# Kernel optimization log

Hardware: AMD Instinct MI355X
Metric: run time of the kernel (lower is better)

## Reference

```python
import jax, jax.numpy as jnp
import numpy as np

N = 20000
E = 640000
IN_DIM = 128
HID = 128
OUT = 64


def setup_inputs() -> dict:
    key = jax.random.key(0)
    ks = jax.random.split(key, 16)
    s = 0.05
    inp = {
        'feat': jax.random.normal(ks[0], (N, IN_DIM), jnp.float32),
        'edge_index': jax.random.randint(ks[1], (2, E), 0, N, jnp.int64),
        # GCNConv params
        'W_gcn': jax.random.normal(ks[2], (IN_DIM, HID), jnp.float32) * s,
        'b_gcn': jnp.zeros((HID,), jnp.float32),
        # SAGEConv params (lin_l: aggregated neighbors w/ bias; lin_r: root, no bias)
        'W_sage_l': jax.random.normal(ks[3], (HID, HID), jnp.float32) * s,
        'b_sage_l': jnp.zeros((HID,), jnp.float32),
        'W_sage_r': jax.random.normal(ks[4], (HID, HID), jnp.float32) * s,
        # policy MLP
        'W1': jax.random.normal(ks[5], (HID, HID), jnp.float32) * s,
        'b1': jnp.zeros((HID,), jnp.float32),
        'W2': jax.random.normal(ks[6], (HID, HID), jnp.float32) * s,
        'b2': jnp.zeros((HID,), jnp.float32),
        'W3': jax.random.normal(ks[7], (HID, OUT), jnp.float32) * s,
        'b3': jnp.zeros((OUT,), jnp.float32),
        # value head
        'Wv': jax.random.normal(ks[8], (HID, 1), jnp.float32) * s,
        'bv': jnp.zeros((1,), jnp.float32),
    }
    return inp


def _gcn(feat, src, dst, W, b):
    # PyG GCNConv: add self loops, sym-normalize by deg^-1/2 on both ends
    loop = jnp.arange(N, dtype=src.dtype)
    s = jnp.concatenate([src, loop])
    d = jnp.concatenate([dst, loop])
    deg = jax.ops.segment_sum(jnp.ones_like(d, jnp.float32), d, num_segments=N)
    dinv = jnp.where(deg > 0, jax.lax.rsqrt(deg), 0.0)
    x = feat @ W  # [N, HID]
    msg = x[s] * (dinv[s] * dinv[d])[:, None]  # [E+N, HID]
    return jax.ops.segment_sum(msg, d, num_segments=N) + b


def _sage_mean(h, src, dst, Wl, bl, Wr):
    # PyG SAGEConv(aggr='mean'): lin_l(mean_neigh) + lin_r(root)
    neigh_sum = jax.ops.segment_sum(h[src], dst, num_segments=N)
    cnt = jax.ops.segment_sum(jnp.ones_like(dst, jnp.float32), dst, num_segments=N)
    mean = neigh_sum / jnp.maximum(cnt, 1.0)[:, None]
    return mean @ Wl + bl + h @ Wr


def reference(feat, edge_index, W_gcn, b_gcn, W_sage_l, b_sage_l, W_sage_r,
              W1, b1, W2, b2, W3, b3, Wv, bv):
    src, dst = edge_index[0], edge_index[1]
    h = jax.nn.relu(_gcn(feat, src, dst, W_gcn, b_gcn))
    h = jax.nn.relu(_sage_mean(h, src, dst, W_sage_l, b_sage_l, W_sage_r))
    # policy MLP (GELU exact, matching torch nn.GELU default)
    z = jax.nn.gelu(h @ W1 + b1, approximate=False)
    z = jax.nn.gelu(z @ W2 + b2, approximate=False)
    means = z @ W3 + b3  # [N, OUT]
    values = (h @ Wv + bv)[:, 0]  # [N]
    return (means, values)
```

## Files before the change

kernel.cpp:

```cpp
#include <hip/hip_runtime.h>
#include <math.h>


typedef __attribute__((ext_vector_type(8))) short short8;
typedef __attribute__((ext_vector_type(4))) float floatx4;

__device__ __forceinline__ unsigned short f2b(float f) {
    unsigned u = __float_as_uint(f);
    unsigned r = (u + 0x7fffu + ((u >> 16) & 1u)) >> 16;
    return (unsigned short)r;
}
__device__ __forceinline__ float b2f(unsigned short h) {
    return __uint_as_float(((unsigned)h) << 16);
}
__device__ __forceinline__ float b2f_lo(unsigned v) {
    return __uint_as_float(v << 16);
}
__device__ __forceinline__ float b2f_hi(unsigned v) {
    return __uint_as_float(v & 0xffff0000u);
}
__device__ __forceinline__ floatx4 MFMA(short8 a, short8 b, floatx4 c) {
    return __builtin_amdgcn_mfma_f32_16x16x32_bf16(a, b, c, 0, 0, 0);
}
__device__ __forceinline__ float gelu_exact(float x) {
    return 0.5f * x * (1.0f + erff(x * 0.70710678118654752440f));
}

#define FRAG(P, ct, ks, lane) (*(const short8*)((P) + (((((ct)*4 + (ks))*64) + (lane)) << 3)))


__global__ __launch_bounds__(256) void count_pack_kernel(
    const int* __restrict__ eidx, int E,
    int* __restrict__ cnt, int* __restrict__ rank,
    const float* Wg, const float* Wsl, const float* Wsr,
    const float* W1, const float* W2, const float* W3,
    unsigned short* Pg, unsigned short* Psl, unsigned short* Psr,
    unsigned short* P1, unsigned short* P2, unsigned short* P3,
    int countBlocks)
{
    if ((int)blockIdx.x < countBlocks) {
        int e = blockIdx.x * 256 + threadIdx.x;
        if (e < E) {
            int d = eidx[E + e];
            rank[e] = atomicAdd(&cnt[d], 1);
        }
        return;
    }
    int t = (blockIdx.x - countBlocks) * 256 + threadIdx.x;
    const float* W; unsigned short* P; int NC = 128; int base;
    if (t < 2048)       { W = Wg;  P = Pg;  base = t; }
    else if (t < 4096)  { W = Wsl; P = Psl; base = t - 2048; }
    else if (t < 6144)  { W = Wsr; P = Psr; base = t - 4096; }
    else if (t < 8192)  { W = W1;  P = P1;  base = t - 6144; }
    else if (t < 10240) { W = W2;  P = P2;  base = t - 8192; }
    else if (t < 11264) { W = W3;  P = P3;  base = t - 10240; NC = 64; }
    else return;
    int l  = base & 63;
    int ks = (base >> 6) & 3;
    int ct = base >> 8;
    int n  = ct * 16 + (l & 15);
    int k0 = ks * 32 + ((l >> 4) << 3);
    short8 v;
    #pragma unroll
    for (int j = 0; j < 8; j++) v[j] = (short)f2b(W[(size_t)(k0 + j) * NC + n]);
    *(short8*)(P + ((size_t)base << 3)) = v;
}


__global__ __launch_bounds__(256) void scan_kernel(
    const int* __restrict__ cnt, int N,
    int* __restrict__ row_ptr, int* __restrict__ bsums,
    float* __restrict__ dinv)
{
    __shared__ int sh[256];
    int b = blockIdx.x, tid = threadIdx.x;
    int i0 = b * 1024 + tid * 4;
    int v0 = (i0 + 0 < N) ? cnt[i0 + 0] : 0;
    int v1 = (i0 + 1 < N) ? cnt[i0 + 1] : 0;
    int v2 = (i0 + 2 < N) ? cnt[i0 + 2] : 0;
    int v3 = (i0 + 3 < N) ? cnt[i0 + 3] : 0;
    int tot = v0 + v1 + v2 + v3;
    sh[tid] = tot;
    __syncthreads();
    for (int off = 1; off < 256; off <<= 1) {
        int t = (tid >= off) ? sh[tid - off] : 0;
        __syncthreads();
        sh[tid] += t;
        __syncthreads();
    }
    int excl = sh[tid] - tot;
    if (i0 + 0 < N) { row_ptr[i0 + 0] = excl;                dinv[i0 + 0] = rsqrtf((float)(v0 + 1)); }
    if (i0 + 1 < N) { row_ptr[i0 + 1] = excl + v0;           dinv[i0 + 1] = rsqrtf((float)(v1 + 1)); }
    if (i0 + 2 < N) { row_ptr[i0 + 2] = excl + v0 + v1;      dinv[i0 + 2] = rsqrtf((float)(v2 + 1)); }
    if (i0 + 3 < N) { row_ptr[i0 + 3] = excl + v0 + v1 + v2; dinv[i0 + 3] = rsqrtf((float)(v3 + 1)); }
    if (tid == 255) bsums[b] = sh[255];
}


__global__ __launch_bounds__(256) void fill_gemm_kernel(
    const int* __restrict__ eidx, const int* __restrict__ rank,
    const int* __restrict__ row_ptr, const int* __restrict__ bsums,
    int E, int* __restrict__ col,
    const float* __restrict__ feat, const unsigned short* __restrict__ Pg,
    unsigned short* __restrict__ xs, int M, int fillBlocks)
{
    if ((int)blockIdx.x < fillBlocks) {
        int e = blockIdx.x * 256 + threadIdx.x;
        if (e < E) {
            int d = eidx[E + e];
            int b = d >> 10;
            int off = 0;
            for (int j = 0; j < b; j++) off += bsums[j];
            col[off + row_ptr[d] + rank[e]] = eidx[e];
        }
        return;
    }
    int bid = blockIdx.x - fillBlocks;
    int w = bid * 4 + (threadIdx.x >> 6);
    if (w >= (M / 16) * 2) return;
    int lane = threadIdx.x & 63;
    int m = lane & 15, quad = lane >> 4;
    int rt = w >> 1, ch = w & 1;
    const float* arow = feat + (size_t)(rt * 16 + m) * 128;
    short8 a[4];
    #pragma unroll
    for (int ks = 0; ks < 4; ks++) {
        float4 f0 = *(const float4*)(arow + ks * 32 + quad * 8);
        float4 f1 = *(const float4*)(arow + ks * 32 + quad * 8 + 4);
        short8 s;
        s[0] = (short)f2b(f0.x); s[1] = (short)f2b(f0.y);
        s[2] = (short)f2b(f0.z); s[3] = (short)f2b(f0.w);
        s[4] = (short)f2b(f1.x); s[5] = (short)f2b(f1.y);
        s[6] = (short)f2b(f1.z); s[7] = (short)f2b(f1.w);
        a[ks] = s;
    }
    #pragma unroll
    for (int ct = 0; ct < 4; ct++) {
        floatx4 acc = {0.f, 0.f, 0.f, 0.f};
        #pragma unroll
        for (int ks = 0; ks < 4; ks++)
            acc = MFMA(a[ks], FRAG(Pg, ch * 4 + ct, ks, lane), acc);
        #pragma unroll
        for (int reg = 0; reg < 4; reg++)
            xs[(size_t)(rt * 16 + quad * 4 + reg) * 128 + (ch * 4 + ct) * 16 + m] =
                f2b(acc[reg]);
    }
}


template<bool GCN>
__global__ __launch_bounds__(256) void agg_kernel(
    const unsigned short* __restrict__ X, const int* __restrict__ row_ptr,
    const int* __restrict__ bsums, const int* __restrict__ col,
    const float* __restrict__ dinv, const float* __restrict__ bias,
    unsigned short* __restrict__ Y, int N, int E)
{
    int w = (int)((blockIdx.x * 256 + threadIdx.x) >> 6);
    if (w >= N) return;
    int lane = threadIdx.x & 63;
    int g = lane >> 4, t = lane & 15;
    const uint4* Xq = (const uint4*)X;

    int b = w >> 10;
    int off = 0;
    for (int j = 0; j < b; j++) off += bsums[j];
    int beg = off + row_ptr[w];
    int end;
    if (w + 1 < N) {
        int off2 = (((w + 1) >> 10) != b) ? off + bsums[b] : off;
        end = off2 + row_ptr[w + 1];
    } else end = E;
    int deg = end - beg;

    float acc[8] = {0.f, 0.f, 0.f, 0.f, 0.f, 0.f, 0.f, 0.f};

    for (int base = beg; base < end; base += 64) {
        int rem = end - base;
        int n = rem < 64 ? rem : 64;
        int idx = (lane < n) ? col[base + lane] : 0;
        for (int j0 = 0; j0 < n; j0 += 16) {
            #pragma unroll
            for (int u = 0; u < 4; u++) {
                int j = j0 + u * 4 + g;
                int s = __shfl(idx, j & 63);
                if (j < n) {
                    uint4 q = Xq[(size_t)s * 16 + t];
                    float sc = GCN ? dinv[s] : 1.0f;
                    acc[0] = fmaf(b2f_lo(q.x), sc, acc[0]);
                    acc[1] = fmaf(b2f_hi(q.x), sc, acc[1]);
                    acc[2] = fmaf(b2f_lo(q.y), sc, acc[2]);
                    acc[3] = fmaf(b2f_hi(q.y), sc, acc[3]);
                    acc[4] = fmaf(b2f_lo(q.z), sc, acc[4]);
                    acc[5] = fmaf(b2f_hi(q.z), sc, acc[5]);
                    acc[6] = fmaf(b2f_lo(q.w), sc, acc[6]);
                    acc[7] = fmaf(b2f_hi(q.w), sc, acc[7]);
                }
            }
        }
    }
    #pragma unroll
    for (int i = 0; i < 8; i++) {
        acc[i] += __shfl_xor(acc[i], 16);
        acc[i] += __shfl_xor(acc[i], 32);
    }
    if (g == 0) {
        float out[8];
        if (GCN) {
            float dw = dinv[w];
            uint4 q = Xq[(size_t)w * 16 + t];
            acc[0] = fmaf(b2f_lo(q.x), dw, acc[0]);
            acc[1] = fmaf(b2f_hi(q.x), dw, acc[1]);
            acc[2] = fmaf(b2f_lo(q.y), dw, acc[2]);
            acc[3] = fmaf(b2f_hi(q.y), dw, acc[3]);
            acc[4] = fmaf(b2f_lo(q.z), dw, acc[4]);
            acc[5] = fmaf(b2f_hi(q.z), dw, acc[5]);
            acc[6] = fmaf(b2f_lo(q.w), dw, acc[6]);
            acc[7] = fmaf(b2f_hi(q.w), dw, acc[7]);
            float4 b0 = *(const float4*)(bias + t * 8);
            float4 b1 = *(const float4*)(bias + t * 8 + 4);
            out[0] = fmaxf(fmaf(acc[0], dw, b0.x), 0.f);
            out[1] = fmaxf(fmaf(acc[1], dw, b0.y), 0.f);
            out[2] = fmaxf(fmaf(acc[2], dw, b0.z), 0.f);
            out[3] = fmaxf(fmaf(acc[3], dw, b0.w), 0.f);
            out[4] = fmaxf(fmaf(acc[4], dw, b1.x), 0.f);
            out[5] = fmaxf(fmaf(acc[5], dw, b1.y), 0.f);
            out[6] = fmaxf(fmaf(acc[6], dw, b1.z), 0.f);
            out[7] = fmaxf(fmaf(acc[7], dw, b1.w), 0.f);
        } else {
            float rc = 1.0f / (float)(deg > 0 ? deg : 1);
            #pragma unroll
            for (int i = 0; i < 8; i++) out[i] = acc[i] * rc;
        }
        uint4 r;
        r.x = (unsigned)f2b(out[0]) | ((unsigned)f2b(out[1]) << 16);
        r.y = (unsigned)f2b(out[2]) | ((unsigned)f2b(out[3]) << 16);
        r.z = (unsigned)f2b(out[4]) | ((unsigned)f2b(out[5]) << 16);
        r.w = (unsigned)f2b(out[6]) | ((unsigned)f2b(out[7]) << 16);
        ((uint4*)Y)[(size_t)w * 16 + t] = r;
    }
}


__global__ __launch_bounds__(256) void sage_mlp_kernel(
    const unsigned short* __restrict__ mean, const unsigned short* __restrict__ h1,
    const unsigned short* __restrict__ Psl, const unsigned short* __restrict__ Psr,
    const float* __restrict__ bsl,
    const unsigned short* __restrict__ P1, const float* __restrict__ b1,
    const unsigned short* __restrict__ P2, const float* __restrict__ b2,
    const unsigned short* __restrict__ P3, const float* __restrict__ b3,
    const float* __restrict__ Wv, const float* __restrict__ bv,
    float* __restrict__ means, float* __restrict__ values, int M)
{
    __shared__ unsigned short z[4][16 * 136];
    int widx = threadIdx.x >> 6, lane = threadIdx.x & 63;
    int w = blockIdx.x * 4 + widx;
    if (w >= M / 16) return;
    int m = lane & 15, quad = lane >> 4;
    unsigned short* zt = &z[widx][0];
    int r0 = w * 16;

    short8 am[4], ar[4];
    #pragma unroll
    for (int ks = 0; ks < 4; ks++) {
        am[ks] = *(const short8*)(mean + (size_t)(r0 + m) * 128 + ks * 32 + quad * 8);
        ar[ks] = *(const short8*)(h1   + (size_t)(r0 + m) * 128 + ks * 32 + quad * 8);
    }

    float vpart[4] = {0.f, 0.f, 0.f, 0.f};
    #pragma unroll
    for (int ct = 0; ct < 8; ct++) {
        floatx4 acc = {0.f, 0.f, 0.f, 0.f};
        #pragma unroll
        for (int ks = 0; ks < 4; ks++) acc = MFMA(am[ks], FRAG(Psl, ct, ks, lane), acc);
        #pragma unroll
        for (int ks = 0; ks < 4; ks++) acc = MFMA(ar[ks], FRAG(Psr, ct, ks, lane), acc);
        float bb = bsl[ct * 16 + m];
        float wv = Wv[ct * 16 + m];
        #pragma unroll
        for (int reg = 0; reg < 4; reg++) {
            float o = fmaxf(acc[reg] + bb, 0.f);
            vpart[reg] = fmaf(o, wv, vpart[reg]);
            zt[(quad * 4 + reg) * 136 + ct * 16 + m] = f2b(o);
        }
    }
    #pragma unroll
    for (int off = 1; off <= 8; off <<= 1) {
        #pragma unroll
        for (int reg = 0; reg < 4; reg++)
            vpart[reg] += __shfl_xor(vpart[reg], off);
    }
    if (m == 0) {
        float bvv = bv[0];
        #pragma unroll
        for (int reg = 0; reg < 4; reg++)
            values[r0 + quad * 4 + reg] = vpart[reg] + bvv;
    }

    short8 a1[4];
    #pragma unroll
    for (int ks = 0; ks < 4; ks++)
        a1[ks] = *(const short8*)(zt + m * 136 + ks * 32 + quad * 8);

    #pragma unroll
    for (int ct = 0; ct < 8; ct++) {
        floatx4 acc = {0.f, 0.f, 0.f, 0.f};
        #pragma unroll
        for (int ks = 0; ks < 4; ks++) acc = MFMA(a1[ks], FRAG(P1, ct, ks, lane), acc);
        float bb = b1[ct * 16 + m];
        #pragma unroll
        for (int reg = 0; reg < 4; reg++)
            zt[(quad * 4 + reg) * 136 + ct * 16 + m] = f2b(gelu_exact(acc[reg] + bb));
    }
    short8 a2[4];
    #pragma unroll
    for (int ks = 0; ks < 4; ks++)
        a2[ks] = *(const short8*)(zt + m * 136 + ks * 32 + quad * 8);

    #pragma unroll
    for (int ct = 0; ct < 8; ct++) {
        floatx4 acc = {0.f, 0.f, 0.f, 0.f};
        #pragma unroll
        for (int ks = 0; ks < 4; ks++) acc = MFMA(a2[ks], FRAG(P2, ct, ks, lane), acc);
        float bb = b2[ct * 16 + m];
        #pragma unroll
        for (int reg = 0; reg < 4; reg++)
            zt[(quad * 4 + reg) * 136 + ct * 16 + m] = f2b(gelu_exact(acc[reg] + bb));
    }
    short8 a3[4];
    #pragma unroll
    for (int ks = 0; ks < 4; ks++)
        a3[ks] = *(const short8*)(zt + m * 136 + ks * 32 + quad * 8);

    #pragma unroll
    for (int ct = 0; ct < 4; ct++) {
        floatx4 acc = {0.f, 0.f, 0.f, 0.f};
        #pragma unroll
        for (int ks = 0; ks < 4; ks++) acc = MFMA(a3[ks], FRAG(P3, ct, ks, lane), acc);
        float bb = b3[ct * 16 + m];
        #pragma unroll
        for (int reg = 0; reg < 4; reg++)
            means[(size_t)(r0 + quad * 4 + reg) * 64 + ct * 16 + m] = acc[reg] + bb;
    }
}


extern "C" void kernel_launch(void* const* d_in, const int* in_sizes, int n_in,
                              void* d_out, int out_size, void* d_ws, size_t ws_size,
                              hipStream_t stream) {
    const float* feat  = (const float*)d_in[0];
    const int*   eidx  = (const int*)d_in[1];
    const float* W_gcn = (const float*)d_in[2];
    const float* b_gcn = (const float*)d_in[3];
    const float* W_sl  = (const float*)d_in[4];
    const float* b_sl  = (const float*)d_in[5];
    const float* W_sr  = (const float*)d_in[6];
    const float* W1    = (const float*)d_in[7];
    const float* b1    = (const float*)d_in[8];
    const float* W2    = (const float*)d_in[9];
    const float* b2    = (const float*)d_in[10];
    const float* W3    = (const float*)d_in[11];
    const float* b3    = (const float*)d_in[12];
    const float* Wv    = (const float*)d_in[13];
    const float* bv    = (const float*)d_in[14];

    const int N = in_sizes[0] / 128;
    const int E = in_sizes[1] / 2;

    char* ws = (char*)d_ws;
    size_t off = 0;
    auto alloc = [&](size_t bytes) -> void* {
        void* p = ws + off;
        off += (bytes + 255) & ~(size_t)255;
        return p;
    };
    int*   cnt     = (int*)alloc((size_t)N * 4);
    int*   rank    = (int*)alloc((size_t)E * 4);
    int*   row_ptr = (int*)alloc((size_t)N * 4);
    int*   bsums   = (int*)alloc(32 * 4);
    float* dinv    = (float*)alloc((size_t)N * 4);
    int*   col     = (int*)alloc((size_t)E * 4);
    unsigned short* xs   = (unsigned short*)alloc((size_t)N * 128 * 2);
    unsigned short* h1   = (unsigned short*)alloc((size_t)N * 128 * 2);
    unsigned short* mean = (unsigned short*)alloc((size_t)N * 128 * 2);
    unsigned short* Pg   = (unsigned short*)alloc(2048 * 8 * 2);
    unsigned short* Psl  = (unsigned short*)alloc(2048 * 8 * 2);
    unsigned short* Psr  = (unsigned short*)alloc(2048 * 8 * 2);
    unsigned short* P1   = (unsigned short*)alloc(2048 * 8 * 2);
    unsigned short* P2   = (unsigned short*)alloc(2048 * 8 * 2);
    unsigned short* P3   = (unsigned short*)alloc(1024 * 8 * 2);

    hipMemsetAsync(cnt, 0, (size_t)N * 4, stream);

    const int countBlocks = (E + 255) / 256;
    const int packBlocks  = (11264 + 255) / 256;
    count_pack_kernel<<<countBlocks + packBlocks, 256, 0, stream>>>(
        eidx, E, cnt, rank, W_gcn, W_sl, W_sr, W1, W2, W3,
        Pg, Psl, Psr, P1, P2, P3, countBlocks);

    const int NB = (N + 1023) / 1024;
    scan_kernel<<<NB, 256, 0, stream>>>(cnt, N, row_ptr, bsums, dinv);

    const int fillBlocks = (E + 255) / 256;
    const int gemmBlocks = ((N / 16) * 2 + 3) / 4;
    fill_gemm_kernel<<<fillBlocks + gemmBlocks, 256, 0, stream>>>(
        eidx, rank, row_ptr, bsums, E, col, feat, Pg, xs, N, fillBlocks);

    const int agrid = (N + 3) / 4;
    agg_kernel<true><<<agrid, 256, 0, stream>>>(xs, row_ptr, bsums, col, dinv, b_gcn, h1, N, E);
    agg_kernel<false><<<agrid, 256, 0, stream>>>(h1, row_ptr, bsums, col, dinv, nullptr, mean, N, E);

    sage_mlp_kernel<<<(N / 16 + 3) / 4, 256, 0, stream>>>(
        mean, h1, Psl, Psr, b_sl, P1, b1, P2, b2, P3, b3, Wv, bv,
        (float*)d_out, (float*)d_out + (size_t)N * 64, N);
}
```

Before: 200.5 us.

## Rework CSR build with decoupled scan, partitioned atomic fill, prescaled GCN features

The per-edge rank array is replaced by atomic write pointers during CSR fill. The fill is partitioned into 8 destination ranges so that each block's atomics hit a localized region. The scan now uses a decoupled lookback with global flags to produce absolute row_ptr, which removes the bsums prefix loops in fill and aggregation. GCN features are prescaled by dinv[src] in the GEMM, so aggregation does plain adds with four independent gathers per iteration. The costs are that the fill reads the edge list 8 times and the column order within each row becomes nondeterministic. The scan's spin-wait also relies on earlier blocks making forward progress.

```diff
diff --git a/kernel.cpp b/kernel.cpp
--- a/kernel.cpp
+++ b/kernel.cpp
@@ -10,9 +10,6 @@
     unsigned r = (u + 0x7fffu + ((u >> 16) & 1u)) >> 16;
     return (unsigned short)r;
 }
-__device__ __forceinline__ float b2f(unsigned short h) {
-    return __uint_as_float(((unsigned)h) << 16);
-}
 __device__ __forceinline__ float b2f_lo(unsigned v) {
     return __uint_as_float(v << 16);
 }
@@ -30,8 +27,7 @@
 
 
 __global__ __launch_bounds__(256) void count_pack_kernel(
-    const int* __restrict__ eidx, int E,
-    int* __restrict__ cnt, int* __restrict__ rank,
+    const int* __restrict__ eidx, int E, int* __restrict__ cnt,
     const float* Wg, const float* Wsl, const float* Wsr,
     const float* W1, const float* W2, const float* W3,
     unsigned short* Pg, unsigned short* Psl, unsigned short* Psr,
@@ -40,10 +36,7 @@
 {
     if ((int)blockIdx.x < countBlocks) {
         int e = blockIdx.x * 256 + threadIdx.x;
-        if (e < E) {
-            int d = eidx[E + e];
-            rank[e] = atomicAdd(&cnt[d], 1);
-        }
+        if (e < E) atomicAdd(&cnt[eidx[E + e]], 1);
         return;
     }
     int t = (blockIdx.x - countBlocks) * 256 + threadIdx.x;
@@ -69,10 +62,11 @@
 
 __global__ __launch_bounds__(256) void scan_kernel(
     const int* __restrict__ cnt, int N,
-    int* __restrict__ row_ptr, int* __restrict__ bsums,
-    float* __restrict__ dinv)
+    int* __restrict__ row_ptr, int* __restrict__ wptr, float* __restrict__ dinv,
+    int* __restrict__ gflags, int* __restrict__ gsums)
 {
     __shared__ int sh[256];
+    __shared__ int s_off;
     int b = blockIdx.x, tid = threadIdx.x;
     int i0 = b * 1024 + tid * 4;
     int v0 = (i0 + 0 < N) ? cnt[i0 + 0] : 0;
@@ -88,30 +82,51 @@
         sh[tid] += t;
         __syncthreads();
     }
-    int excl = sh[tid] - tot;
-    if (i0 + 0 < N) { row_ptr[i0 + 0] = excl;                dinv[i0 + 0] = rsqrtf((float)(v0 + 1)); }
-    if (i0 + 1 < N) { row_ptr[i0 + 1] = excl + v0;           dinv[i0 + 1] = rsqrtf((float)(v1 + 1)); }
-    if (i0 + 2 < N) { row_ptr[i0 + 2] = excl + v0 + v1;      dinv[i0 + 2] = rsqrtf((float)(v2 + 1)); }
-    if (i0 + 3 < N) { row_ptr[i0 + 3] = excl + v0 + v1 + v2; dinv[i0 + 3] = rsqrtf((float)(v3 + 1)); }
-    if (tid == 255) bsums[b] = sh[255];
+    if (tid == 255) {
+        gsums[b] = sh[255];
+        __hip_atomic_store(&gflags[b], 1, __ATOMIC_RELEASE, __HIP_MEMORY_SCOPE_AGENT);
+    }
+    if (tid == 0) {
+        int off = 0;
+        for (int j = 0; j < b; j++) {
+            while (__hip_atomic_load(&gflags[j], __ATOMIC_ACQUIRE,
+                                     __HIP_MEMORY_SCOPE_AGENT) == 0) {}
+            off += gsums[j];
+        }
+        s_off = off;
+    }
+    __syncthreads();
+    int excl = s_off + sh[tid] - tot;
+    if (i0 + 0 < N) { row_ptr[i0 + 0] = excl;                wptr[i0 + 0] = excl;                dinv[i0 + 0] = rsqrtf((float)(v0 + 1)); }
+    if (i0 + 1 < N) { row_ptr[i0 + 1] = excl + v0;           wptr[i0 + 1] = excl + v0;           dinv[i0 + 1] = rsqrtf((float)(v1 + 1)); }
+    if (i0 + 2 < N) { row_ptr[i0 + 2] = excl + v0 + v1;      wptr[i0 + 2] = excl + v0 + v1;      dinv[i0 + 2] = rsqrtf((float)(v2 + 1)); }
+    if (i0 + 3 < N) { row_ptr[i0 + 3] = excl + v0 + v1 + v2; wptr[i0 + 3] = excl + v0 + v1 + v2; dinv[i0 + 3] = rsqrtf((float)(v3 + 1)); }
+    if (b == (int)gridDim.x - 1 && tid == 255) row_ptr[N] = s_off + sh[255];
 }
 
 
 __global__ __launch_bounds__(256) void fill_gemm_kernel(
-    const int* __restrict__ eidx, const int* __restrict__ rank,
-    const int* __restrict__ row_ptr, const int* __restrict__ bsums,
-    int E, int* __restrict__ col,
-    const float* __restrict__ feat, const unsigned short* __restrict__ Pg,
-    unsigned short* __restrict__ xs, int M, int fillBlocks)
+    const int* __restrict__ eidx, int E, int N,
+    int* __restrict__ wptr, int* __restrict__ col,
+    const float* __restrict__ feat, const float* __restrict__ dinv,
+    const unsigned short* __restrict__ Pg, unsigned short* __restrict__ xs,
+    int M, int fillBlocks, int PS)
 {
     if ((int)blockIdx.x < fillBlocks) {
-        int e = blockIdx.x * 256 + threadIdx.x;
-        if (e < E) {
-            int d = eidx[E + e];
-            int b = d >> 10;
-            int off = 0;
-            for (int j = 0; j < b; j++) off += bsums[j];
-            col[off + row_ptr[d] + rank[e]] = eidx[e];
+        int p = blockIdx.x & 7;
+        int chunk = blockIdx.x >> 3;
+        int dlo = p * PS;
+        int dhi = dlo + PS; if (dhi > N) dhi = N;
+        #pragma unroll
+        for (int it = 0; it < 8; it++) {
+            int e = (chunk * 8 + it) * 256 + threadIdx.x;
+            if (e < E) {
+                int d = eidx[E + e];
+                if (d >= dlo && d < dhi) {
+                    int pos = atomicAdd(&wptr[d], 1);
+                    col[pos] = eidx[e];
+                }
+            }
         }
         return;
     }
@@ -134,6 +149,9 @@
         s[6] = (short)f2b(f1.z); s[7] = (short)f2b(f1.w);
         a[ks] = s;
     }
+    float dvr[4];
+    #pragma unroll
+    for (int reg = 0; reg < 4; reg++) dvr[reg] = dinv[rt * 16 + quad * 4 + reg];
     #pragma unroll
     for (int ct = 0; ct < 4; ct++) {
         floatx4 acc = {0.f, 0.f, 0.f, 0.f};
@@ -143,59 +161,50 @@
         #pragma unroll
         for (int reg = 0; reg < 4; reg++)
             xs[(size_t)(rt * 16 + quad * 4 + reg) * 128 + (ch * 4 + ct) * 16 + m] =
-                f2b(acc[reg]);
-    }
-}
-
+                f2b(acc[reg] * dvr[reg]);
+    }
+}
+
+
+#define ACCUM(q)                                   \
+    acc[0] += b2f_lo((q).x); acc[1] += b2f_hi((q).x); \
+    acc[2] += b2f_lo((q).y); acc[3] += b2f_hi((q).y); \
+    acc[4] += b2f_lo((q).z); acc[5] += b2f_hi((q).z); \
+    acc[6] += b2f_lo((q).w); acc[7] += b2f_hi((q).w);
 
 template<bool GCN>
 __global__ __launch_bounds__(256) void agg_kernel(
     const unsigned short* __restrict__ X, const int* __restrict__ row_ptr,
-    const int* __restrict__ bsums, const int* __restrict__ col,
-    const float* __restrict__ dinv, const float* __restrict__ bias,
-    unsigned short* __restrict__ Y, int N, int E)
+    const int* __restrict__ col, const float* __restrict__ dinv,
+    const float* __restrict__ bias, unsigned short* __restrict__ Y, int N)
 {
     int w = (int)((blockIdx.x * 256 + threadIdx.x) >> 6);
     if (w >= N) return;
     int lane = threadIdx.x & 63;
     int g = lane >> 4, t = lane & 15;
     const uint4* Xq = (const uint4*)X;
-
-    int b = w >> 10;
-    int off = 0;
-    for (int j = 0; j < b; j++) off += bsums[j];
-    int beg = off + row_ptr[w];
-    int end;
-    if (w + 1 < N) {
-        int off2 = (((w + 1) >> 10) != b) ? off + bsums[b] : off;
-        end = off2 + row_ptr[w + 1];
-    } else end = E;
+    int beg = row_ptr[w], end = row_ptr[w + 1];
     int deg = end - beg;
 
     float acc[8] = {0.f, 0.f, 0.f, 0.f, 0.f, 0.f, 0.f, 0.f};
-
-    for (int base = beg; base < end; base += 64) {
-        int rem = end - base;
-        int n = rem < 64 ? rem : 64;
-        int idx = (lane < n) ? col[base + lane] : 0;
-        for (int j0 = 0; j0 < n; j0 += 16) {
-            #pragma unroll
-            for (int u = 0; u < 4; u++) {
-                int j = j0 + u * 4 + g;
-                int s = __shfl(idx, j & 63);
-                if (j < n) {
-                    uint4 q = Xq[(size_t)s * 16 + t];
-                    float sc = GCN ? dinv[s] : 1.0f;
-                    acc[0] = fmaf(b2f_lo(q.x), sc, acc[0]);
-                    acc[1] = fmaf(b2f_hi(q.x), sc, acc[1]);
-                    acc[2] = fmaf(b2f_lo(q.y), sc, acc[2]);
-                    acc[3] = fmaf(b2f_hi(q.y), sc, acc[3]);
-                    acc[4] = fmaf(b2f_lo(q.z), sc, acc[4]);
-                    acc[5] = fmaf(b2f_hi(q.z), sc, acc[5]);
-                    acc[6] = fmaf(b2f_lo(q.w), sc, acc[6]);
-                    acc[7] = fmaf(b2f_hi(q.w), sc, acc[7]);
-                }
-            }
+    int jb = beg;
+    for (; jb + 16 <= end; jb += 16) {
+        int s0 = col[jb + g];
+        int s1 = col[jb + g + 4];
+        int s2 = col[jb + g + 8];
+        int s3 = col[jb + g + 12];
+        uint4 q0 = Xq[(size_t)s0 * 16 + t];
+        uint4 q1 = Xq[(size_t)s1 * 16 + t];
+        uint4 q2 = Xq[(size_t)s2 * 16 + t];
+        uint4 q3 = Xq[(size_t)s3 * 16 + t];
+        ACCUM(q0) ACCUM(q1) ACCUM(q2) ACCUM(q3)
+    }
+    for (; jb < end; jb += 4) {
+        int j = jb + g;
+        if (j < end) {
+            int s = col[j];
+            uint4 q = Xq[(size_t)s * 16 + t];
+            ACCUM(q)
         }
     }
     #pragma unroll
@@ -206,16 +215,9 @@
     if (g == 0) {
         float out[8];
         if (GCN) {
+            uint4 q = Xq[(size_t)w * 16 + t];
+            ACCUM(q)
             float dw = dinv[w];
-            uint4 q = Xq[(size_t)w * 16 + t];
-            acc[0] = fmaf(b2f_lo(q.x), dw, acc[0]);
-            acc[1] = fmaf(b2f_hi(q.x), dw, acc[1]);
-            acc[2] = fmaf(b2f_lo(q.y), dw, acc[2]);
-            acc[3] = fmaf(b2f_hi(q.y), dw, acc[3]);
-            acc[4] = fmaf(b2f_lo(q.z), dw, acc[4]);
-            acc[5] = fmaf(b2f_hi(q.z), dw, acc[5]);
-            acc[6] = fmaf(b2f_lo(q.w), dw, acc[6]);
-            acc[7] = fmaf(b2f_hi(q.w), dw, acc[7]);
             float4 b0 = *(const float4*)(bias + t * 8);
             float4 b1 = *(const float4*)(bias + t * 8 + 4);
             out[0] = fmaxf(fmaf(acc[0], dw, b0.x), 0.f);
@@ -373,10 +375,12 @@
         off += (bytes + 255) & ~(size_t)255;
         return p;
     };
-    int*   cnt     = (int*)alloc((size_t)N * 4);
-    int*   rank    = (int*)alloc((size_t)E * 4);
-    int*   row_ptr = (int*)alloc((size_t)N * 4);
-    int*   bsums   = (int*)alloc(32 * 4);
+    int*   gflags  = (int*)alloc((size_t)(64 + N) * 4);
+    int*   cnt     = gflags + 64;
+    size_t zbytes  = (size_t)(64 + N) * 4;
+    int*   gsums   = (int*)alloc(64 * 4);
+    int*   row_ptr = (int*)alloc((size_t)(N + 1) * 4);
+    int*   wptr    = (int*)alloc((size_t)N * 4);
     float* dinv    = (float*)alloc((size_t)N * 4);
     int*   col     = (int*)alloc((size_t)E * 4);
     unsigned short* xs   = (unsigned short*)alloc((size_t)N * 128 * 2);
@@ -389,25 +393,27 @@
     unsigned short* P2   = (unsigned short*)alloc(2048 * 8 * 2);
     unsigned short* P3   = (unsigned short*)alloc(1024 * 8 * 2);
 
-    hipMemsetAsync(cnt, 0, (size_t)N * 4, stream);
+    hipMemsetAsync(gflags, 0, zbytes, stream);
 
     const int countBlocks = (E + 255) / 256;
     const int packBlocks  = (11264 + 255) / 256;
     count_pack_kernel<<<countBlocks + packBlocks, 256, 0, stream>>>(
-        eidx, E, cnt, rank, W_gcn, W_sl, W_sr, W1, W2, W3,
+        eidx, E, cnt, W_gcn, W_sl, W_sr, W1, W2, W3,
         Pg, Psl, Psr, P1, P2, P3, countBlocks);
 
     const int NB = (N + 1023) / 1024;
-    scan_kernel<<<NB, 256, 0, stream>>>(cnt, N, row_ptr, bsums, dinv);
-
-    const int fillBlocks = (E + 255) / 256;
+    scan_kernel<<<NB, 256, 0, stream>>>(cnt, N, row_ptr, wptr, dinv, gflags, gsums);
+
+    const int PS = (N + 7) / 8;
+    const int chunks = (E + 2047) / 2048;
+    const int fillBlocks = chunks * 8;
     const int gemmBlocks = ((N / 16) * 2 + 3) / 4;
     fill_gemm_kernel<<<fillBlocks + gemmBlocks, 256, 0, stream>>>(
-        eidx, rank, row_ptr, bsums, E, col, feat, Pg, xs, N, fillBlocks);
+        eidx, E, N, wptr, col, feat, dinv, Pg, xs, N, fillBlocks, PS);
 
     const int agrid = (N + 3) / 4;
-    agg_kernel<true><<<agrid, 256, 0, stream>>>(xs, row_ptr, bsums, col, dinv, b_gcn, h1, N, E);
-    agg_kernel<false><<<agrid, 256, 0, stream>>>(h1, row_ptr, bsums, col, dinv, nullptr, mean, N, E);
+    agg_kernel<true><<<agrid, 256, 0, stream>>>(xs, row_ptr, col, dinv, b_gcn, h1, N);
+    agg_kernel<false><<<agrid, 256, 0, stream>>>(h1, row_ptr, col, dinv, nullptr, mean, N);
 
     sage_mlp_kernel<<<(N / 16 + 3) / 4, 256, 0, stream>>>(
         mean, h1, Psl, Psr, b_sl, P1, b1, P2, b2, P3, b3, Wv, bv,
```

Result: slower. 221.0 us (+10.2%).
